# Kernel tuning notes

Hardware: AMD Instinct MI355X
Metric: run time of the kernel (lower is better)

Reference implementation:

```python
import jax, jax.numpy as jnp
import numpy as np

N = 100000   # total nodes
E = 1600000  # edges
F_IN = 128   # num_features
HL1 = 128    # hidden
G = 100      # num graphs
GF = 16      # num_global_feats
GH = 32      # global_hl1 (hardcoded in module)


def _gcn_conv(x, W, b, src, dst, n):
    # PyG GCNConv: add self-loops, symmetric deg^{-1/2} normalization,
    # linear transform then normalized scatter-add aggregation, plus bias.
    h = x @ W  # [n, out]
    ones = jnp.ones(src.shape[0], x.dtype)
    deg = jax.ops.segment_sum(ones, dst, num_segments=n) + 1.0  # +1 for self-loop
    dinv = jnp.where(deg > 0, 1.0 / jnp.sqrt(deg), 0.0)
    norm = dinv[src] * dinv[dst]                      # [E]
    agg = jax.ops.segment_sum(h[src] * norm[:, None], dst, num_segments=n)
    agg = agg + h * (dinv * dinv)[:, None]            # self-loop messages (i->i)
    return agg + b


def setup_inputs() -> dict:
    key = jax.random.key(0)
    ks = jax.random.split(key, 24)
    inp = {}
    inp["x"] = jax.random.normal(ks[0], (N, F_IN), jnp.float32)
    inp["edge_index"] = jax.random.randint(ks[1], (2, E), 0, N, jnp.int64)
    inp["batch"] = jnp.sort(jax.random.randint(ks[2], (N,), 0, G, jnp.int32))
    inp["global_feats"] = jax.random.normal(ks[3], (G * GF,), jnp.float32)
    inp["num_graphs"] = G
    s = 0.05
    inp["conv1_W"] = jax.random.normal(ks[4], (F_IN, HL1), jnp.float32) * s
    inp["conv1_b"] = jnp.zeros((HL1,), jnp.float32)
    inp["conv2_W"] = jax.random.normal(ks[5], (HL1, HL1), jnp.float32) * s
    inp["conv2_b"] = jnp.zeros((HL1,), jnp.float32)
    inp["conv3_W"] = jax.random.normal(ks[6], (HL1, HL1), jnp.float32) * s
    inp["conv3_b"] = jnp.zeros((HL1,), jnp.float32)
    inp["conv4_W"] = jax.random.normal(ks[7], (HL1, HL1), jnp.float32) * s
    inp["conv4_b"] = jnp.zeros((HL1,), jnp.float32)
    inp["global1_W"] = jax.random.normal(ks[8], (GF, GH), jnp.float32) * s
    inp["global1_b"] = jnp.zeros((GH,), jnp.float32)
    inp["lin1_W"] = jax.random.normal(ks[9], (HL1, HL1), jnp.float32) * s
    inp["lin1_b"] = jnp.zeros((HL1,), jnp.float32)
    inp["lin2_W"] = jax.random.normal(ks[10], (HL1 + GH, HL1), jnp.float32) * s
    inp["lin2_b"] = jnp.zeros((HL1,), jnp.float32)
    inp["lin3_W"] = jax.random.normal(ks[11], (HL1, HL1), jnp.float32) * s
    inp["lin3_b"] = jnp.zeros((HL1,), jnp.float32)
    inp["lin4_W"] = jax.random.normal(ks[12], (HL1, 1), jnp.float32) * s
    inp["lin4_b"] = jnp.zeros((1,), jnp.float32)
    return inp


def reference(x, edge_index, batch, global_feats, num_graphs,
              conv1_W, conv1_b, conv2_W, conv2_b, conv3_W, conv3_b,
              conv4_W, conv4_b, global1_W, global1_b,
              lin1_W, lin1_b, lin2_W, lin2_b, lin3_W, lin3_b, lin4_W, lin4_b):
    src, dst = edge_index[0], edge_index[1]
    n = x.shape[0]
    relu = jax.nn.relu
    h = relu(_gcn_conv(x, conv1_W, conv1_b, src, dst, n))
    h = relu(_gcn_conv(h, conv2_W, conv2_b, src, dst, n))
    h = relu(_gcn_conv(h, conv3_W, conv3_b, src, dst, n))
    h = relu(_gcn_conv(h, conv4_W, conv4_b, src, dst, n))
    # per-graph sum pooling (vectorized segment-sum instead of python loop)
    pooled = jax.ops.segment_sum(h, batch, num_segments=num_graphs)  # [G, HL1]
    gfs = global_feats.reshape(num_graphs, -1)                        # [G, GF]
    g = relu(gfs @ global1_W + global1_b)                             # [G, GH]
    y = relu(pooled @ lin1_W + lin1_b)
    y = jnp.concatenate([y, g], axis=1)
    y = relu(y @ lin2_W + lin2_b)
    y = relu(y @ lin3_W + lin3_b)
    y = y @ lin4_W + lin4_b
    return y.squeeze(1)  # final_act == 'none'
```

## Files before the change

kernel.cpp:

```cpp
#include <hip/hip_runtime.h>
#include <hip/hip_bf16.h>

#define NN 100000
#define NE 1600000
#define FD 128
#define NG 100
#define GFD 16
#define GHD 32

#define NB 391
#define BCAP 5120

typedef __attribute__((ext_vector_type(8))) _Float16 f16x8;
typedef __attribute__((ext_vector_type(2))) _Float16 f16x2;
typedef __attribute__((ext_vector_type(4))) float f32x4;

static inline int cdiv(int a, int b) { return (a + b - 1) / b; }


__global__ void k_zero_int(int* __restrict__ p, int n) {
  int i = blockIdx.x * blockDim.x + threadIdx.x;
  if (i < n) p[i] = 0;
}

__global__ __launch_bounds__(256) void k_binA(const int* __restrict__ src,
                                              const int* __restrict__ dst,
                                              int* __restrict__ gcur,
                                              unsigned int* __restrict__ stag) {
  __shared__ int cnt[NB];
  __shared__ int gbase[NB];
  __shared__ int cursor[NB];
  int t = threadIdx.x;
  for (int i = t; i < NB; i += 256) cnt[i] = 0;
  __syncthreads();
  int e0 = blockIdx.x * 2048;
  int s[8], d[8], b[8];
#pragma unroll
  for (int j = 0; j < 8; j++) {
    int e = e0 + j * 256 + t;
    if (e < NE) {
      s[j] = src[e];
      d[j] = dst[e];
      b[j] = d[j] >> 8;
      atomicAdd(&cnt[b[j]], 1);
    } else {
      b[j] = -1;
    }
  }
  __syncthreads();
  for (int i = t; i < NB; i += 256) {
    int c = cnt[i];
    gbase[i] = (c > 0) ? atomicAdd(&gcur[i], c) : 0;
    cursor[i] = 0;
  }
  __syncthreads();
#pragma unroll
  for (int j = 0; j < 8; j++) {
    if (b[j] >= 0) {
      int r = atomicAdd(&cursor[b[j]], 1);
      stag[(size_t)b[j] * BCAP + gbase[b[j]] + r] =
          ((unsigned int)s[j] << 8) | (unsigned int)(d[j] & 255);
    }
  }
}

__global__ __launch_bounds__(256) void k_binB(const unsigned int* __restrict__ stag,
                                              const int* __restrict__ gcur,
                                              int* __restrict__ deg,
                                              float* __restrict__ dinv) {
  __shared__ int h[256];
  int b = blockIdx.x;
  int t = threadIdx.x;
  h[t] = 0;
  __syncthreads();
  int n = gcur[b];
  const unsigned int* p = stag + (size_t)b * BCAP;
  for (int i = t; i < n; i += 256) atomicAdd(&h[p[i] & 255], 1);
  __syncthreads();
  int node = b * 256 + t;
  if (node < NN) {
    int dg = h[t];
    deg[node] = dg;
    dinv[node] = 1.0f / sqrtf((float)(dg + 1));
  }
}

__global__ __launch_bounds__(256) void k_scan1(const int* __restrict__ deg,
                                               int* __restrict__ offs,
                                               int* __restrict__ bsum) {
  __shared__ int sh[256];
  int b = blockIdx.x;
  int t = threadIdx.x;
  int base = b * 1024 + t * 4;
  int v0 = (base + 0 < NN) ? deg[base + 0] : 0;
  int v1 = (base + 1 < NN) ? deg[base + 1] : 0;
  int v2 = (base + 2 < NN) ? deg[base + 2] : 0;
  int v3 = (base + 3 < NN) ? deg[base + 3] : 0;
  int s = v0 + v1 + v2 + v3;
  sh[t] = s;
  __syncthreads();
  for (int off = 1; off < 256; off <<= 1) {
    int tv = (t >= off) ? sh[t - off] : 0;
    __syncthreads();
    sh[t] += tv;
    __syncthreads();
  }
  int excl = sh[t] - s;
  if (base + 0 < NN) offs[base + 0] = excl;
  if (base + 1 < NN) offs[base + 1] = excl + v0;
  if (base + 2 < NN) offs[base + 2] = excl + v0 + v1;
  if (base + 3 < NN) offs[base + 3] = excl + v0 + v1 + v2;
  if (t == 255) bsum[b] = sh[255];
}

__global__ __launch_bounds__(128) void k_scan2(int* __restrict__ bsum, int nb) {
  __shared__ int sh[128];
  int t = threadIdx.x;
  int v = (t < nb) ? bsum[t] : 0;
  sh[t] = v;
  __syncthreads();
  for (int off = 1; off < 128; off <<= 1) {
    int tv = (t >= off) ? sh[t - off] : 0;
    __syncthreads();
    sh[t] += tv;
    __syncthreads();
  }
  if (t < nb) bsum[t] = sh[t] - v;
}

__global__ void k_scan3(int* __restrict__ offs, const int* __restrict__ bsum) {
  int i = blockIdx.x * blockDim.x + threadIdx.x;
  if (i < NN) offs[i] = offs[i] + bsum[i >> 10];
  if (i == 0) offs[NN] = NE;
}

__global__ __launch_bounds__(256) void k_binC(const unsigned int* __restrict__ stag,
                                              const int* __restrict__ gcur,
                                              const int* __restrict__ offs,
                                              int* __restrict__ ssrc) {
  __shared__ int cur[256];
  int b = blockIdx.x;
  int t = threadIdx.x;
  int node = b * 256 + t;
  cur[t] = (node < NN) ? offs[node] : 0;
  __syncthreads();
  int n = gcur[b];
  const unsigned int* p = stag + (size_t)b * BCAP;
  for (int i = t; i < n; i += 256) {
    unsigned int v = p[i];
    int pos = atomicAdd(&cur[v & 255], 1);
    ssrc[pos] = (int)(v >> 8);
  }
}


__global__ void k_cvt_x(const float* __restrict__ X, _Float16* __restrict__ Xh) {
  int i = blockIdx.x * blockDim.x + threadIdx.x;
  if (i >= NN * FD / 8) return;
  const float4* src = (const float4*)(X + (size_t)i * 8);
  float4 a = src[0], b = src[1];
  f16x8 o = {(_Float16)a.x, (_Float16)a.y, (_Float16)a.z, (_Float16)a.w,
             (_Float16)b.x, (_Float16)b.y, (_Float16)b.z, (_Float16)b.w};
  *(f16x8*)(Xh + (size_t)i * 8) = o;
}

__global__ void k_cvt_w(const float* __restrict__ W, _Float16* __restrict__ Wf) {
  int t = blockIdx.x * blockDim.x + threadIdx.x;
  if (t >= 16384) return;
  int i = t & 7;
  int l = (t >> 3) & 63;
  int nt = (t >> 9) & 7;
  int kb = (t >> 12) & 3;
  int k = kb * 32 + (l >> 4) * 8 + i;
  int n = nt * 16 + (l & 15);
  float w = W[k * FD + n];
  _Float16 hi = (_Float16)w;
  Wf[t] = hi;
  Wf[t + 16384] = (_Float16)(w - (float)hi);
}

__global__ __launch_bounds__(256) void k_gemm_mfma(
    const _Float16* __restrict__ Xh,
    const _Float16* __restrict__ Wfrag,
    const float* __restrict__ dinv,
    _Float16* __restrict__ Hs) {
  int tid = threadIdx.x;
  int lane = tid & 63;
  int wave = tid >> 6;
  int r0 = blockIdx.x * 64 + wave * 16;
  int arow = r0 + (lane & 15);
  int kgrp = lane >> 4;

  f32x4 acc[8];
#pragma unroll
  for (int nt = 0; nt < 8; nt++) acc[nt] = (f32x4){0.f, 0.f, 0.f, 0.f};

#pragma unroll
  for (int kb = 0; kb < 4; kb++) {
    f16x8 a;
    if (arow < NN) {
      a = *(const f16x8*)(Xh + (size_t)arow * FD + kb * 32 + kgrp * 8);
    } else {
      a = (f16x8){0, 0, 0, 0, 0, 0, 0, 0};
    }
    const _Float16* wp = Wfrag + ((size_t)(kb * 8) * 64 + lane) * 8;
#pragma unroll
    for (int nt = 0; nt < 8; nt++) {
      f16x8 bhi = *(const f16x8*)(wp + (size_t)nt * 64 * 8);
      f16x8 blo = *(const f16x8*)(wp + (size_t)nt * 64 * 8 + 16384);
      acc[nt] = __builtin_amdgcn_mfma_f32_16x16x32_f16(a, bhi, acc[nt], 0, 0, 0);
      acc[nt] = __builtin_amdgcn_mfma_f32_16x16x32_f16(a, blo, acc[nt], 0, 0, 0);
    }
  }

  int ccol = lane & 15;
  int rbase = r0 + (lane >> 4) * 4;
  float dv[4];
#pragma unroll
  for (int j = 0; j < 4; j++) dv[j] = (rbase + j < NN) ? dinv[rbase + j] : 0.f;
#pragma unroll
  for (int nt = 0; nt < 8; nt++) {
#pragma unroll
    for (int j = 0; j < 4; j++) {
      int r = rbase + j;
      if (r < NN) {
        Hs[(size_t)r * FD + nt * 16 + ccol] = (_Float16)(acc[nt][j] * dv[j]);
      }
    }
  }
}

__global__ __launch_bounds__(256) void k_agg(const _Float16* __restrict__ Hs,
                                             const float* __restrict__ dinv,
                                             const int* __restrict__ offs,
                                             const int* __restrict__ ssrc,
                                             const float* __restrict__ bias,
                                             _Float16* __restrict__ Bout) {
  int wave = threadIdx.x >> 6;
  int lane = threadIdx.x & 63;
  int node = blockIdx.x * 4 + wave;
  float di = dinv[node];
  f16x2 sv = *(const f16x2*)(Hs + (size_t)node * FD + lane * 2);
  float acc0 = (float)sv.x, acc1 = (float)sv.y;
  int e0 = offs[node], e1 = offs[node + 1];
  int e = e0;
  for (; e + 4 <= e1; e += 4) {
    int s0 = ssrc[e], s1 = ssrc[e + 1], s2 = ssrc[e + 2], s3 = ssrc[e + 3];
    f16x2 v0 = *(const f16x2*)(Hs + (size_t)s0 * FD + lane * 2);
    f16x2 v1 = *(const f16x2*)(Hs + (size_t)s1 * FD + lane * 2);
    f16x2 v2 = *(const f16x2*)(Hs + (size_t)s2 * FD + lane * 2);
    f16x2 v3 = *(const f16x2*)(Hs + (size_t)s3 * FD + lane * 2);
    acc0 += (float)v0.x + (float)v1.x + (float)v2.x + (float)v3.x;
    acc1 += (float)v0.y + (float)v1.y + (float)v2.y + (float)v3.y;
  }
  for (; e < e1; e++) {
    int s = ssrc[e];
    f16x2 hv = *(const f16x2*)(Hs + (size_t)s * FD + lane * 2);
    acc0 += (float)hv.x;
    acc1 += (float)hv.y;
  }
  float2 bv = *(const float2*)(bias + lane * 2);
  f16x2 o;
  o.x = (_Float16)fmaxf(fmaf(acc0, di, bv.x), 0.f);
  o.y = (_Float16)fmaxf(fmaf(acc1, di, bv.y), 0.f);
  *(f16x2*)(Bout + (size_t)node * FD + lane * 2) = o;
}

__global__ __launch_bounds__(128) void k_pool(const _Float16* __restrict__ H,
                                              const int* __restrict__ batch,
                                              float* __restrict__ part) {
  int g = blockIdx.x >> 3;
  int s = blockIdx.x & 7;
  int start, end;
  {
    int lo = 0, hi = NN;
    while (lo < hi) { int m = (lo + hi) >> 1; if (batch[m] < g) lo = m + 1; else hi = m; }
    start = lo;
    lo = start; hi = NN;
    while (lo < hi) { int m = (lo + hi) >> 1; if (batch[m] < g + 1) lo = m + 1; else hi = m; }
    end = lo;
  }
  int cnt = end - start;
  int chunk = (cnt + 7) >> 3;
  int a = start + s * chunk;
  int bnd = a + chunk;
  if (bnd > end) bnd = end;
  int f = threadIdx.x;
  float acc = 0.f;
  for (int i = a; i < bnd; i++) acc += (float)H[(size_t)i * FD + f];
  part[(size_t)blockIdx.x * FD + f] = acc;
}

__global__ __launch_bounds__(128) void k_tail(
    const float* __restrict__ part, const float* __restrict__ gfeats,
    const float* __restrict__ W1, const float* __restrict__ b1,
    const float* __restrict__ Wg, const float* __restrict__ bg,
    const float* __restrict__ W2, const float* __restrict__ b2,
    const float* __restrict__ W3, const float* __restrict__ b3,
    const float* __restrict__ W4, const float* __restrict__ b4,
    float* __restrict__ out) {
  __shared__ float row[FD];
  __shared__ float y1[FD];
  __shared__ float gv[GHD];
  __shared__ float y2[FD];
  __shared__ float red[FD];
  int g = blockIdx.x, j = threadIdx.x;

  float p = 0.f;
  for (int s = 0; s < 8; s++) p += part[(size_t)(g * 8 + s) * FD + j];
  row[j] = p;
  if (j < GHD) {
    float a = bg[j];
    for (int k = 0; k < GFD; k++) a = fmaf(gfeats[g * GFD + k], Wg[k * GHD + j], a);
    gv[j] = fmaxf(a, 0.f);
  }
  __syncthreads();

  float a1 = b1[j];
  for (int k = 0; k < FD; k++) a1 = fmaf(row[k], W1[k * FD + j], a1);
  y1[j] = fmaxf(a1, 0.f);
  __syncthreads();

  float a2 = b2[j];
  for (int k = 0; k < FD; k++) a2 = fmaf(y1[k], W2[k * FD + j], a2);
  for (int k = 0; k < GHD; k++) a2 = fmaf(gv[k], W2[(FD + k) * FD + j], a2);
  y2[j] = fmaxf(a2, 0.f);
  __syncthreads();

  float a3 = b3[j];
  for (int k = 0; k < FD; k++) a3 = fmaf(y2[k], W3[k * FD + j], a3);
  float y3 = fmaxf(a3, 0.f);

  red[j] = y3 * W4[j];
  __syncthreads();
  for (int st = 64; st > 0; st >>= 1) {
    if (j < st) red[j] += red[j + st];
    __syncthreads();
  }
  if (j == 0) out[g] = red[0] + b4[0];
}

extern "C" void kernel_launch(void* const* d_in, const int* in_sizes, int n_in,
                              void* d_out, int out_size, void* d_ws, size_t ws_size,
                              hipStream_t stream) {
  const float* x      = (const float*)d_in[0];
  const int*   ei     = (const int*)d_in[1];
  const int*   batch  = (const int*)d_in[2];
  const float* gfeats = (const float*)d_in[3];
  const float* c1W = (const float*)d_in[5];  const float* c1b = (const float*)d_in[6];
  const float* c2W = (const float*)d_in[7];  const float* c2b = (const float*)d_in[8];
  const float* c3W = (const float*)d_in[9];  const float* c3b = (const float*)d_in[10];
  const float* c4W = (const float*)d_in[11]; const float* c4b = (const float*)d_in[12];
  const float* gW  = (const float*)d_in[13]; const float* gb  = (const float*)d_in[14];
  const float* l1W = (const float*)d_in[15]; const float* l1b = (const float*)d_in[16];
  const float* l2W = (const float*)d_in[17]; const float* l2b = (const float*)d_in[18];
  const float* l3W = (const float*)d_in[19]; const float* l3b = (const float*)d_in[20];
  const float* l4W = (const float*)d_in[21]; const float* l4b = (const float*)d_in[22];
  const int* srcp = ei;
  const int* dstp = ei + NE;
  float* out = (float*)d_out;

  char* p = (char*)d_ws;
  auto alloc = [&](size_t bytes) {
    char* r = p;
    p += (bytes + 255) & ~(size_t)255;
    return (void*)r;
  };
  _Float16* Xh  = (_Float16*)alloc((size_t)NN * FD * 2);
  _Float16* Hs  = (_Float16*)alloc((size_t)NN * FD * 2);
  _Float16* Bb  = (_Float16*)alloc((size_t)NN * FD * 2);
  _Float16* Wf0 = (_Float16*)alloc(32768 * 2);
  _Float16* Wf1 = (_Float16*)alloc(32768 * 2);
  _Float16* Wf2 = (_Float16*)alloc(32768 * 2);
  _Float16* Wf3 = (_Float16*)alloc(32768 * 2);
  float* dinv = (float*)alloc((size_t)NN * 4);
  int*   deg  = (int*)alloc((size_t)NN * 4);
  int*   offs = (int*)alloc((size_t)(NN + 1) * 4);
  int*   ssrc = (int*)alloc((size_t)NE * 4);
  int*   bsum = (int*)alloc(128 * 4);
  float* part = (float*)alloc((size_t)NG * 8 * FD * 4);
  unsigned int* stag = (unsigned int*)alloc((size_t)NB * BCAP * 4);
  int*   gcur = (int*)alloc((size_t)NB * 4);

  int nb_scan = cdiv(NN, 1024);

  k_zero_int<<<cdiv(NB, 256), 256, 0, stream>>>(gcur, NB);
  k_binA<<<cdiv(NE, 2048), 256, 0, stream>>>(srcp, dstp, gcur, stag);
  k_binB<<<NB, 256, 0, stream>>>(stag, gcur, deg, dinv);
  k_scan1<<<nb_scan, 256, 0, stream>>>(deg, offs, bsum);
  k_scan2<<<1, 128, 0, stream>>>(bsum, nb_scan);
  k_scan3<<<cdiv(NN, 256), 256, 0, stream>>>(offs, bsum);
  k_binC<<<NB, 256, 0, stream>>>(stag, gcur, offs, ssrc);

  k_cvt_x<<<cdiv(NN * FD / 8, 256), 256, 0, stream>>>(x, Xh);
  k_cvt_w<<<64, 256, 0, stream>>>(c1W, Wf0);
  k_cvt_w<<<64, 256, 0, stream>>>(c2W, Wf1);
  k_cvt_w<<<64, 256, 0, stream>>>(c3W, Wf2);
  k_cvt_w<<<64, 256, 0, stream>>>(c4W, Wf3);

  int gemm_grid = cdiv(NN, 64);
  const _Float16* Xin = Xh;
  const _Float16* Wfs[4] = {Wf0, Wf1, Wf2, Wf3};
  const float* bs4[4] = {c1b, c2b, c3b, c4b};
  for (int l = 0; l < 4; l++) {
    k_gemm_mfma<<<gemm_grid, 256, 0, stream>>>(Xin, Wfs[l], dinv, Hs);
    k_agg<<<NN / 4, 256, 0, stream>>>(Hs, dinv, offs, ssrc, bs4[l], Bb);
    Xin = Bb;
  }

  k_pool<<<NG * 8, 128, 0, stream>>>(Bb, batch, part);
  k_tail<<<NG, 128, 0, stream>>>(part, gfeats, l1W, l1b, gW, gb, l2W, l2b,
                                 l3W, l3b, l4W, l4b, out);
}
```

Before: 547.4 us.

## Pad CSR rows to multiples of 8 and fuse fp32-to-fp16 input conversion into first GEMM

Each node's neighbor list is padded to a multiple of 8 with a dummy source index pointing to an all-zero extra row of Hs. This lets the aggregation kernel load 16-byte f16x8 vectors, with four lane groups each handling two edges per step, and combine partial sums through cross-lane shuffles. This replaces the narrow 4-byte-per-lane gathers with wider memory transactions. The separate x conversion kernel is removed and the first-layer GEMM reads the fp32 input directly. The trade-off is extra padded edges, which add loads and index storage, and wasted lanes on low-degree nodes.

```diff
diff --git a/kernel.cpp b/kernel.cpp
--- a/kernel.cpp
+++ b/kernel.cpp
@@ -21,6 +21,11 @@
 __global__ void k_zero_int(int* __restrict__ p, int n) {
   int i = blockIdx.x * blockDim.x + threadIdx.x;
   if (i < n) p[i] = 0;
+}
+
+__global__ void k_zero_row(_Float16* __restrict__ Hs) {
+  int t = threadIdx.x;
+  if (t < FD) Hs[(size_t)NN * FD + t] = (_Float16)0.f;
 }
 
 __global__ __launch_bounds__(256) void k_binA(const int* __restrict__ src,
@@ -92,10 +97,10 @@
   int b = blockIdx.x;
   int t = threadIdx.x;
   int base = b * 1024 + t * 4;
-  int v0 = (base + 0 < NN) ? deg[base + 0] : 0;
-  int v1 = (base + 1 < NN) ? deg[base + 1] : 0;
-  int v2 = (base + 2 < NN) ? deg[base + 2] : 0;
-  int v3 = (base + 3 < NN) ? deg[base + 3] : 0;
+  int v0 = (base + 0 < NN) ? ((deg[base + 0] + 7) & ~7) : 0;
+  int v1 = (base + 1 < NN) ? ((deg[base + 1] + 7) & ~7) : 0;
+  int v2 = (base + 2 < NN) ? ((deg[base + 2] + 7) & ~7) : 0;
+  int v3 = (base + 3 < NN) ? ((deg[base + 3] + 7) & ~7) : 0;
   int s = v0 + v1 + v2 + v3;
   sh[t] = s;
   __syncthreads();
@@ -113,7 +118,8 @@
   if (t == 255) bsum[b] = sh[255];
 }
 
-__global__ __launch_bounds__(128) void k_scan2(int* __restrict__ bsum, int nb) {
+__global__ __launch_bounds__(128) void k_scan2(int* __restrict__ bsum, int nb,
+                                               int* __restrict__ ptot) {
   __shared__ int sh[128];
   int t = threadIdx.x;
   int v = (t < nb) ? bsum[t] : 0;
@@ -126,12 +132,14 @@
     __syncthreads();
   }
   if (t < nb) bsum[t] = sh[t] - v;
-}
-
-__global__ void k_scan3(int* __restrict__ offs, const int* __restrict__ bsum) {
+  if (t == nb - 1) ptot[0] = sh[t];
+}
+
+__global__ void k_scan3(int* __restrict__ offs, const int* __restrict__ bsum,
+                        const int* __restrict__ ptot) {
   int i = blockIdx.x * blockDim.x + threadIdx.x;
   if (i < NN) offs[i] = offs[i] + bsum[i >> 10];
-  if (i == 0) offs[NN] = NE;
+  if (i == 0) offs[NN] = ptot[0];
 }
 
 __global__ __launch_bounds__(256) void k_binC(const unsigned int* __restrict__ stag,
@@ -151,18 +159,13 @@
     int pos = atomicAdd(&cur[v & 255], 1);
     ssrc[pos] = (int)(v >> 8);
   }
-}
-
-
-__global__ void k_cvt_x(const float* __restrict__ X, _Float16* __restrict__ Xh) {
-  int i = blockIdx.x * blockDim.x + threadIdx.x;
-  if (i >= NN * FD / 8) return;
-  const float4* src = (const float4*)(X + (size_t)i * 8);
-  float4 a = src[0], b = src[1];
-  f16x8 o = {(_Float16)a.x, (_Float16)a.y, (_Float16)a.z, (_Float16)a.w,
-             (_Float16)b.x, (_Float16)b.y, (_Float16)b.z, (_Float16)b.w};
-  *(f16x8*)(Xh + (size_t)i * 8) = o;
-}
+  __syncthreads();
+  if (node < NN) {
+    int end = offs[node + 1];
+    for (int pos = cur[t]; pos < end; pos++) ssrc[pos] = NN;
+  }
+}
+
 
 __global__ void k_cvt_w(const float* __restrict__ W, _Float16* __restrict__ Wf) {
   int t = blockIdx.x * blockDim.x + threadIdx.x;
@@ -230,6 +233,60 @@
   }
 }
 
+__global__ __launch_bounds__(256) void k_gemm_mfma_f32(
+    const float* __restrict__ X,
+    const _Float16* __restrict__ Wfrag,
+    const float* __restrict__ dinv,
+    _Float16* __restrict__ Hs) {
+  int tid = threadIdx.x;
+  int lane = tid & 63;
+  int wave = tid >> 6;
+  int r0 = blockIdx.x * 64 + wave * 16;
+  int arow = r0 + (lane & 15);
+  int kgrp = lane >> 4;
+
+  f32x4 acc[8];
+#pragma unroll
+  for (int nt = 0; nt < 8; nt++) acc[nt] = (f32x4){0.f, 0.f, 0.f, 0.f};
+
+#pragma unroll
+  for (int kb = 0; kb < 4; kb++) {
+    f16x8 a;
+    if (arow < NN) {
+      const float4* xp = (const float4*)(X + (size_t)arow * FD + kb * 32 + kgrp * 8);
+      float4 x0 = xp[0], x1 = xp[1];
+      a = (f16x8){(_Float16)x0.x, (_Float16)x0.y, (_Float16)x0.z, (_Float16)x0.w,
+                  (_Float16)x1.x, (_Float16)x1.y, (_Float16)x1.z, (_Float16)x1.w};
+    } else {
+      a = (f16x8){0, 0, 0, 0, 0, 0, 0, 0};
+    }
+    const _Float16* wp = Wfrag + ((size_t)(kb * 8) * 64 + lane) * 8;
+#pragma unroll
+    for (int nt = 0; nt < 8; nt++) {
+      f16x8 bhi = *(const f16x8*)(wp + (size_t)nt * 64 * 8);
+      f16x8 blo = *(const f16x8*)(wp + (size_t)nt * 64 * 8 + 16384);
+      acc[nt] = __builtin_amdgcn_mfma_f32_16x16x32_f16(a, bhi, acc[nt], 0, 0, 0);
+      acc[nt] = __builtin_amdgcn_mfma_f32_16x16x32_f16(a, blo, acc[nt], 0, 0, 0);
+    }
+  }
+
+  int ccol = lane & 15;
+  int rbase = r0 + (lane >> 4) * 4;
+  float dv[4];
+#pragma unroll
+  for (int j = 0; j < 4; j++) dv[j] = (rbase + j < NN) ? dinv[rbase + j] : 0.f;
+#pragma unroll
+  for (int nt = 0; nt < 8; nt++) {
+#pragma unroll
+    for (int j = 0; j < 4; j++) {
+      int r = rbase + j;
+      if (r < NN) {
+        Hs[(size_t)r * FD + nt * 16 + ccol] = (_Float16)(acc[nt][j] * dv[j]);
+      }
+    }
+  }
+}
+
 __global__ __launch_bounds__(256) void k_agg(const _Float16* __restrict__ Hs,
                                              const float* __restrict__ dinv,
                                              const int* __restrict__ offs,
@@ -239,31 +296,41 @@
   int wave = threadIdx.x >> 6;
   int lane = threadIdx.x & 63;
   int node = blockIdx.x * 4 + wave;
-  float di = dinv[node];
-  f16x2 sv = *(const f16x2*)(Hs + (size_t)node * FD + lane * 2);
-  float acc0 = (float)sv.x, acc1 = (float)sv.y;
+  int g = lane >> 4;
+  int c = lane & 15;
+
+  float acc[8];
+#pragma unroll
+  for (int k = 0; k < 8; k++) acc[k] = 0.f;
+
   int e0 = offs[node], e1 = offs[node + 1];
-  int e = e0;
-  for (; e + 4 <= e1; e += 4) {
-    int s0 = ssrc[e], s1 = ssrc[e + 1], s2 = ssrc[e + 2], s3 = ssrc[e + 3];
-    f16x2 v0 = *(const f16x2*)(Hs + (size_t)s0 * FD + lane * 2);
-    f16x2 v1 = *(const f16x2*)(Hs + (size_t)s1 * FD + lane * 2);
-    f16x2 v2 = *(const f16x2*)(Hs + (size_t)s2 * FD + lane * 2);
-    f16x2 v3 = *(const f16x2*)(Hs + (size_t)s3 * FD + lane * 2);
-    acc0 += (float)v0.x + (float)v1.x + (float)v2.x + (float)v3.x;
-    acc1 += (float)v0.y + (float)v1.y + (float)v2.y + (float)v3.y;
-  }
-  for (; e < e1; e++) {
-    int s = ssrc[e];
-    f16x2 hv = *(const f16x2*)(Hs + (size_t)s * FD + lane * 2);
-    acc0 += (float)hv.x;
-    acc1 += (float)hv.y;
-  }
-  float2 bv = *(const float2*)(bias + lane * 2);
-  f16x2 o;
-  o.x = (_Float16)fmaxf(fmaf(acc0, di, bv.x), 0.f);
-  o.y = (_Float16)fmaxf(fmaf(acc1, di, bv.y), 0.f);
-  *(f16x2*)(Bout + (size_t)node * FD + lane * 2) = o;
+  for (int e = e0; e < e1; e += 8) {
+    int2 sv = *(const int2*)(ssrc + e + g * 2);
+    f16x8 v0 = *(const f16x8*)(Hs + (size_t)sv.x * FD + c * 8);
+    f16x8 v1 = *(const f16x8*)(Hs + (size_t)sv.y * FD + c * 8);
+#pragma unroll
+    for (int k = 0; k < 8; k++) acc[k] += (float)v0[k] + (float)v1[k];
+  }
+
+#pragma unroll
+  for (int k = 0; k < 8; k++) {
+    acc[k] += __shfl_xor(acc[k], 16, 64);
+    acc[k] += __shfl_xor(acc[k], 32, 64);
+  }
+
+  if (g == 0) {
+    float di = dinv[node];
+    f16x8 sf = *(const f16x8*)(Hs + (size_t)node * FD + c * 8);
+    float4 b0 = *(const float4*)(bias + c * 8);
+    float4 b1 = *(const float4*)(bias + c * 8 + 4);
+    float bb[8] = {b0.x, b0.y, b0.z, b0.w, b1.x, b1.y, b1.z, b1.w};
+    f16x8 o;
+#pragma unroll
+    for (int k = 0; k < 8; k++) {
+      o[k] = (_Float16)fmaxf(fmaf(acc[k] + (float)sf[k], di, bb[k]), 0.f);
+    }
+    *(f16x8*)(Bout + (size_t)node * FD + c * 8) = o;
+  }
 }
 
 __global__ __launch_bounds__(128) void k_pool(const _Float16* __restrict__ H,
@@ -366,8 +433,7 @@
     p += (bytes + 255) & ~(size_t)255;
     return (void*)r;
   };
-  _Float16* Xh  = (_Float16*)alloc((size_t)NN * FD * 2);
-  _Float16* Hs  = (_Float16*)alloc((size_t)NN * FD * 2);
+  _Float16* Hs  = (_Float16*)alloc((size_t)(NN + 1) * FD * 2);
   _Float16* Bb  = (_Float16*)alloc((size_t)NN * FD * 2);
   _Float16* Wf0 = (_Float16*)alloc(32768 * 2);
   _Float16* Wf1 = (_Float16*)alloc(32768 * 2);
@@ -376,8 +442,9 @@
   float* dinv = (float*)alloc((size_t)NN * 4);
   int*   deg  = (int*)alloc((size_t)NN * 4);
   int*   offs = (int*)alloc((size_t)(NN + 1) * 4);
-  int*   ssrc = (int*)alloc((size_t)NE * 4);
+  int*   ssrc = (int*)alloc((size_t)(NE + 8 * NN) * 4);
   int*   bsum = (int*)alloc(128 * 4);
+  int*   ptot = (int*)alloc(256);
   float* part = (float*)alloc((size_t)NG * 8 * FD * 4);
   unsigned int* stag = (unsigned int*)alloc((size_t)NB * BCAP * 4);
   int*   gcur = (int*)alloc((size_t)NB * 4);
@@ -385,27 +452,27 @@
   int nb_scan = cdiv(NN, 1024);
 
   k_zero_int<<<cdiv(NB, 256), 256, 0, stream>>>(gcur, NB);
+  k_zero_row<<<1, 128, 0, stream>>>(Hs);
   k_binA<<<cdiv(NE, 2048), 256, 0, stream>>>(srcp, dstp, gcur, stag);
   k_binB<<<NB, 256, 0, stream>>>(stag, gcur, deg, dinv);
   k_scan1<<<nb_scan, 256, 0, stream>>>(deg, offs, bsum);
-  k_scan2<<<1, 128, 0, stream>>>(bsum, nb_scan);
-  k_scan3<<<cdiv(NN, 256), 256, 0, stream>>>(offs, bsum);
+  k_scan2<<<1, 128, 0, stream>>>(bsum, nb_scan, ptot);
+  k_scan3<<<cdiv(NN, 256), 256, 0, stream>>>(offs, bsum, ptot);
   k_binC<<<NB, 256, 0, stream>>>(stag, gcur, offs, ssrc);
 
-  k_cvt_x<<<cdiv(NN * FD / 8, 256), 256, 0, stream>>>(x, Xh);
   k_cvt_w<<<64, 256, 0, stream>>>(c1W, Wf0);
   k_cvt_w<<<64, 256, 0, stream>>>(c2W, Wf1);
   k_cvt_w<<<64, 256, 0, stream>>>(c3W, Wf2);
   k_cvt_w<<<64, 256, 0, stream>>>(c4W, Wf3);
 
   int gemm_grid = cdiv(NN, 64);
-  const _Float16* Xin = Xh;
   const _Float16* Wfs[4] = {Wf0, Wf1, Wf2, Wf3};
   const float* bs4[4] = {c1b, c2b, c3b, c4b};
-  for (int l = 0; l < 4; l++) {
-    k_gemm_mfma<<<gemm_grid, 256, 0, stream>>>(Xin, Wfs[l], dinv, Hs);
+  k_gemm_mfma_f32<<<gemm_grid, 256, 0, stream>>>(x, Wf0, dinv, Hs);
+  k_agg<<<NN / 4, 256, 0, stream>>>(Hs, dinv, offs, ssrc, bs4[0], Bb);
+  for (int l = 1; l < 4; l++) {
+    k_gemm_mfma<<<gemm_grid, 256, 0, stream>>>(Bb, Wfs[l], dinv, Hs);
     k_agg<<<NN / 4, 256, 0, stream>>>(Hs, dinv, offs, ssrc, bs4[l], Bb);
-    Xin = Bb;
   }
 
   k_pool<<<NG * 8, 128, 0, stream>>>(Bb, batch, part);
```

Result: faster. 502.3 us (-8.2%).
